# Performance work log

Measured on AMD Instinct MI355X. Metric: run time of the kernel, lower is better.

The kernel has to match this reference:

```python
import jax, jax.numpy as jnp
import numpy as np

HEADS = 12
HEAD_SIZE = 64
NEG_BIG = 1e12


def _rope_sin_cos(seq_len, head_size, dtype):
    # embeddings[n, 2i] = sin(n * 10000^(-2i/d)), [n, 2i+1] = cos(...)
    pos = jnp.arange(seq_len, dtype=dtype)                      # [s]
    idx = jnp.arange(head_size // 2, dtype=dtype)               # [d/2]
    inv_freq = jnp.power(jnp.asarray(10000.0, dtype), -2.0 * idx / head_size)
    ang = jnp.einsum('n,d->nd', pos, inv_freq)                  # [s, d/2]
    # cos_pos / sin_pos: repeat_interleave each frequency twice -> [1, s, 1, d]
    cos = jnp.repeat(jnp.cos(ang), 2, axis=-1)[None, :, None, :]
    sin = jnp.repeat(jnp.sin(ang), 2, axis=-1)[None, :, None, :]
    return sin, cos


def _rotate_half_interleaved(x):
    # stack([-x[..., 1::2], x[..., ::2]], -1).reshape_as(x)
    x2 = jnp.stack([-x[..., 1::2], x[..., ::2]], axis=-1)
    return x2.reshape(x.shape)


def setup_inputs() -> dict:
    key = jax.random.key(0)
    k1, k2 = jax.random.split(key)
    bs, s, h = 16, 512, 768
    hidden = jax.random.normal(k1, (bs, s, h), dtype=jnp.float32)
    attention_mask = jnp.ones((bs, s), dtype=jnp.int32)
    W = jax.random.normal(k2, (h, HEADS * 2 * HEAD_SIZE), dtype=jnp.float32) * (h ** -0.5)
    b = jnp.zeros((HEADS * 2 * HEAD_SIZE,), dtype=jnp.float32)
    return {"hidden": hidden, "attention_mask": attention_mask, "W": W, "b": b}


def reference(hidden, attention_mask, W, b):
    bs, s, _ = hidden.shape
    x = hidden @ W + b                                           # [b, s, heads*2*hd]
    x = x.reshape(bs, s, HEADS, 2, HEAD_SIZE)
    qw, kw = x[..., 0, :], x[..., 1, :]                          # [b, s, h, d]

    sin, cos = _rope_sin_cos(s, HEAD_SIZE, hidden.dtype)
    qw = qw * cos + _rotate_half_interleaved(qw) * sin
    kw = kw * cos + _rotate_half_interleaved(kw) * sin

    logits = jnp.einsum('bmhd,bnhd->bhmn', qw, kw)               # [b, h, s, s]

    am = attention_mask.astype(logits.dtype)
    pad_mask = 1.0 - am[:, None, None, :] * am[:, None, :, None]
    logits = logits - pad_mask * NEG_BIG

    tril = jnp.tril(jnp.ones((s, s), dtype=logits.dtype), k=-1)  # strictly lower
    logits = logits - tril[None, None, :, :] * NEG_BIG

    return logits / (HEAD_SIZE ** 0.5)
```

## Files before the change

### kernel.cpp

```cpp
#include <hip/hip_runtime.h>
#include <math.h>

#define HEADS 12
#define HSZ   64
#define SEQ   512
#define HID   768
#define NOUT  1536
#define NEGQ  1.25e11f

typedef _Float16 f16x8 __attribute__((ext_vector_type(8)));
typedef _Float16 f16x4 __attribute__((ext_vector_type(4)));
typedef float    f32x4 __attribute__((ext_vector_type(4)));
typedef int      i32x4 __attribute__((ext_vector_type(4)));
typedef int      i32x8 __attribute__((ext_vector_type(8)));

__device__ __forceinline__ void async_ld16(const void* g, void* l) {
  __builtin_amdgcn_global_load_lds(
      (__attribute__((address_space(1))) void*)g,
      (__attribute__((address_space(3))) void*)l, 16, 0, 0);
}

__global__ __launch_bounds__(256) void prep_k(
    const float* __restrict__ hidden, const float* __restrict__ W,
    unsigned char* __restrict__ Xb8, unsigned char* __restrict__ Wt8,
    float2* __restrict__ tab)
{
  __shared__ float t_lds[32][33];
  const int b = blockIdx.x;
  const int t = threadIdx.x;
  if (b < 1152) {
    const int tk = b % 24, tn = b / 24;
    const int k0 = tk * 32, n0 = tn * 32;
    const int tx = t & 31, ty = t >> 5;
#pragma unroll
    for (int r = 0; r < 4; ++r)
      t_lds[ty + r * 8][tx] = W[(size_t)(k0 + ty + r * 8) * NOUT + n0 + tx];
    __syncthreads();
    const int nl = t >> 3, kg = t & 7;
    int w = __builtin_amdgcn_cvt_pk_fp8_f32(t_lds[kg * 4 + 0][nl],
                                            t_lds[kg * 4 + 1][nl], 0, false);
    w = __builtin_amdgcn_cvt_pk_fp8_f32(t_lds[kg * 4 + 2][nl],
                                        t_lds[kg * 4 + 3][nl], w, true);
    *(int*)&Wt8[(size_t)(n0 + nl) * HID + k0 + kg * 4] = w;
  } else if (b < 1152 + 1536) {
    const int base = (b - 1152) * 1024;
    const float4* src4 = (const float4*)hidden;
    int* dst = (int*)Xb8;
#pragma unroll
    for (int p = 0; p < 4; ++p) {
      const int i = base + p * 256 + t;
      const float4 v = src4[i];
      int o = __builtin_amdgcn_cvt_pk_fp8_f32(v.x, v.y, 0, false);
      o = __builtin_amdgcn_cvt_pk_fp8_f32(v.z, v.w, o, true);
      dst[i] = o;
    }
  } else {
    const int e = (b - 2688) * 256 + t;
    const int si = e >> 5, fi = e & 31;
    float inv = powf(10000.f, -(float)fi / 32.f);
    float ang = (float)si * inv;
    float sv, cv;
    sincosf(ang, &sv, &cv);
    tab[e] = make_float2(cv, sv);
  }
}

__global__ __launch_bounds__(256) void gemm1_k(
    const unsigned char* __restrict__ Xb8, const unsigned char* __restrict__ Wt8,
    const float* __restrict__ bias, const float2* __restrict__ tab,
    const int* __restrict__ am, float* __restrict__ out,
    _Float16* __restrict__ qb, _Float16* __restrict__ kb)
{
  __shared__ __align__(16) int As4[4096];
  __shared__ __align__(16) int Bs4[4096];
  const int tid = threadIdx.x;
  const int blk = blockIdx.x;

  if (blk >= 768) {
    const int idx = blk - 768;
    const int bh = idx / 6, f = idx % 6;
    const int te = (0xEDC984 >> (f * 4)) & 15;
    const int m0 = (te >> 2) * 128, n0 = (te & 3) * 128;
    const int* amb = am + (bh / HEADS) * SEQ;
    float* obase = out + (size_t)bh * SEQ * SEQ;
#pragma unroll
    for (int p = 0; p < 16; ++p) {
      const int ff = p * 256 + tid;
      const int row = ff >> 5, c4 = (ff & 31) * 4;
      const int m = m0 + row;
      const float amm = (float)amb[m];
      const int nb = n0 + c4;
      const int4 a4 = *(const int4*)&amb[nb];
      f32x4 v;
      v[0] = -(2.f - amm * (float)a4.x) * NEGQ;
      v[1] = -(2.f - amm * (float)a4.y) * NEGQ;
      v[2] = -(2.f - amm * (float)a4.z) * NEGQ;
      v[3] = -(2.f - amm * (float)a4.w) * NEGQ;
      __builtin_nontemporal_store(v, (f32x4*)&obase[(size_t)m * SEQ + nb]);
    }
    return;
  }

  const int lane = tid & 63;
  const int m0 = (blk & 63) * 128;
  const int h = blk >> 6;
  const int n0 = h * 128;
  const int wm = ((tid >> 6) & 1) * 64;
  const int wn = (tid >> 7) * 64;
  const int lrow = lane & 15;
  const int q = lane >> 4;

  f32x4 acc[4][4] = {};

#pragma unroll
  for (int c = 0; c < 4; ++c) {
    const int s = tid + c * 256;
    const int row = s >> 3, cc = s & 7;
    const int so = (((cc >> 1) ^ (row & 3)) << 5) + ((cc & 1) << 4);
    async_ld16(Xb8 + (size_t)(m0 + row) * HID + so, (char*)As4 + s * 16);
    async_ld16(Wt8 + (size_t)(n0 + row) * HID + so, (char*)Bs4 + s * 16);
  }

  for (int kt = 0; kt < 6; ++kt) {
    __syncthreads();
    i32x8 af[4], bf[4];
#pragma unroll
    for (int i = 0; i < 4; ++i) {
      const int ra = wm + i * 16 + lrow;
      const int oa = ra * 32 + ((q ^ (ra & 3)) << 3);
      i32x4 lo = *(const i32x4*)&As4[oa];
      i32x4 hi = *(const i32x4*)&As4[oa + 4];
      af[i] = (i32x8){lo.x, lo.y, lo.z, lo.w, hi.x, hi.y, hi.z, hi.w};
      const int rb = wn + i * 16 + lrow;
      const int ob = rb * 32 + ((q ^ (rb & 3)) << 3);
      lo = *(const i32x4*)&Bs4[ob];
      hi = *(const i32x4*)&Bs4[ob + 4];
      bf[i] = (i32x8){lo.x, lo.y, lo.z, lo.w, hi.x, hi.y, hi.z, hi.w};
    }
    __syncthreads();
    if (kt < 5) {
      const int kbase = (kt + 1) * 128;
#pragma unroll
      for (int c = 0; c < 4; ++c) {
        const int s = tid + c * 256;
        const int row = s >> 3, cc = s & 7;
        const int so = (((cc >> 1) ^ (row & 3)) << 5) + ((cc & 1) << 4);
        async_ld16(Xb8 + (size_t)(m0 + row) * HID + kbase + so, (char*)As4 + s * 16);
        async_ld16(Wt8 + (size_t)(n0 + row) * HID + kbase + so, (char*)Bs4 + s * 16);
      }
    }
#pragma unroll
    for (int i = 0; i < 4; ++i)
#pragma unroll
      for (int j = 0; j < 4; ++j)
        acc[i][j] = __builtin_amdgcn_mfma_scale_f32_16x16x128_f8f6f4(
            bf[j], af[i], acc[i][j], 0, 0,
            0, 0x7F7F7F7F, 0, 0x7F7F7F7F);
  }
  __syncthreads();

  {
    const int qlane = lane >> 4;
    const int rbase = wm + (lane & 15);
    f16x4* sdst = wn ? (f16x4*)Bs4 : (f16x4*)As4;
#pragma unroll
    for (int j = 0; j < 4; ++j) {
      const int d0 = j * 16 + qlane * 4;
      const int nb = n0 + wn + d0;
      const float4 b4 = *(const float4*)&bias[nb];
      const int fi0 = d0 >> 1;
#pragma unroll
      for (int i = 0; i < 4; ++i) {
        const int r = rbase + i * 16;
        const int m = m0 + r;
        const int si = m & (SEQ - 1);
        const float4 cs = *(const float4*)&tab[si * 32 + fi0];
        const float v0 = acc[i][j][0] + b4.x;
        const float v1 = acc[i][j][1] + b4.y;
        const float v2 = acc[i][j][2] + b4.z;
        const float v3 = acc[i][j][3] + b4.w;
        f16x4 o;
        o.x = (_Float16)fmaf(v0, cs.x, -v1 * cs.y);
        o.y = (_Float16)fmaf(v1, cs.x, v0 * cs.y);
        o.z = (_Float16)fmaf(v2, cs.z, -v3 * cs.w);
        o.w = (_Float16)fmaf(v3, cs.z, v2 * cs.w);
        sdst[r * 16 + ((d0 >> 2) ^ ((r & 7) << 1))] = o;
      }
    }
  }
  __syncthreads();

  {
    const int bb = m0 >> 9;
    const int si0 = m0 & (SEQ - 1);
    _Float16* qdst = qb + ((size_t)(bb * HEADS + h) * SEQ + si0) * HSZ;
    _Float16* kdst = kb + ((size_t)(bb * HEADS + h) * SEQ + si0) * HSZ;
#pragma unroll
    for (int p = 0; p < 4; ++p) {
      const int idx = p * 256 + tid;
      const int row = idx >> 3, v = idx & 7;
      const int sv = v ^ (row & 7);
      f16x8 qv = ((const f16x8*)As4)[row * 8 + sv];
      f16x8 kv = ((const f16x8*)Bs4)[row * 8 + sv];
      *(f16x8*)(qdst + row * HSZ + v * 8) = qv;
      *(f16x8*)(kdst + row * HSZ + v * 8) = kv;
    }
  }
}

__global__ __launch_bounds__(256) void gemm2_k(
    const _Float16* __restrict__ qb, const _Float16* __restrict__ kb,
    const int* __restrict__ am, float* __restrict__ out)
{
  __shared__ __align__(16) float sbuf[64 * 128];
  const int tid = threadIdx.x;
  const int blk = blockIdx.x;
  const int xcd = blk & 7;
  const int slot = blk >> 3;
  const int bh = xcd * 24 + slot / 10;
  const int bb = bh / HEADS;
  const int te = (int)((0xFBA7653210ULL >> ((slot % 10) * 4)) & 15);
  const int mt = te >> 2, nt = te & 3;
  const int m0 = mt * 128, n0 = nt * 128;
  const int* amb = am + bb * SEQ;
  float* obase = out + (size_t)bh * SEQ * SEQ;

  const _Float16* qg = qb + (size_t)bh * SEQ * HSZ;
  const _Float16* kg = kb + (size_t)bh * SEQ * HSZ;
  const int lane = tid & 63;
  const int wm = ((tid >> 6) & 1) * 64;
  const int wn = (tid >> 7) * 64;
  const int lrow = lane & 15;
  const int lk = (lane >> 4) * 8;

  f16x8 af[4][2], bf[4][2];
#pragma unroll
  for (int i = 0; i < 4; ++i)
#pragma unroll
    for (int h = 0; h < 2; ++h) {
      af[i][h] = *(const f16x8*)(qg + (size_t)(m0 + wm + i * 16 + lrow) * HSZ + h * 32 + lk);
      bf[i][h] = *(const f16x8*)(kg + (size_t)(n0 + wn + i * 16 + lrow) * HSZ + h * 32 + lk);
    }

  f32x4 acc[4][4] = {};
#pragma unroll
  for (int h = 0; h < 2; ++h)
#pragma unroll
    for (int i = 0; i < 4; ++i)
#pragma unroll
      for (int j = 0; j < 4; ++j)
        acc[i][j] = __builtin_amdgcn_mfma_f32_16x16x32_f16(bf[j][h], af[i][h], acc[i][j], 0, 0, 0);

  const int qlane = lane >> 4;
  const int rloc = lane & 15;
  const int wmp = wm >> 6;
  for (int ph = 0; ph < 2; ++ph) {
    if (wmp == ph) {
#pragma unroll
      for (int i = 0; i < 4; ++i) {
        const int r = i * 16 + rloc;
        const int m = m0 + wm + r;
        const float amm = (float)amb[m];
#pragma unroll
        for (int j = 0; j < 4; ++j) {
          const int nb = n0 + wn + j * 16 + qlane * 4;
          const int4 a4 = *(const int4*)&amb[nb];
          f32x4 v;
          v[0] = fmaf(acc[i][j][0], 0.125f,
                      -((float)(nb + 0 < m) + (1.f - amm * (float)a4.x)) * NEGQ);
          v[1] = fmaf(acc[i][j][1], 0.125f,
                      -((float)(nb + 1 < m) + (1.f - amm * (float)a4.y)) * NEGQ);
          v[2] = fmaf(acc[i][j][2], 0.125f,
                      -((float)(nb + 2 < m) + (1.f - amm * (float)a4.z)) * NEGQ);
          v[3] = fmaf(acc[i][j][3], 0.125f,
                      -((float)(nb + 3 < m) + (1.f - amm * (float)a4.w)) * NEGQ);
          const int t = ((wn >> 2) + j * 4 + qlane) ^ (r & 7);
          *(f32x4*)&sbuf[r * 128 + t * 4] = v;
        }
      }
    }
    __syncthreads();
    const int rowbase = m0 + ph * 64;
#pragma unroll
    for (int p = 0; p < 8; ++p) {
      const int idx = p * 256 + tid;
      const int row = idx >> 5, t = idx & 31;
      f32x4 v = *(const f32x4*)&sbuf[row * 128 + ((t ^ (row & 7)) * 4)];
      __builtin_nontemporal_store(
          v, (f32x4*)&obase[(size_t)(rowbase + row) * SEQ + n0 + t * 4]);
    }
    __syncthreads();
  }
}

extern "C" void kernel_launch(void* const* d_in, const int* in_sizes, int n_in,
                              void* d_out, int out_size, void* d_ws, size_t ws_size,
                              hipStream_t stream) {
  const float* hidden = (const float*)d_in[0];
  const int*   am     = (const int*)d_in[1];
  const float* W      = (const float*)d_in[2];
  const float* bias   = (const float*)d_in[3];
  float* out = (float*)d_out;
  char* ws = (char*)d_ws;
  unsigned char* Xb8 = (unsigned char*)(ws);
  unsigned char* Wt8 = (unsigned char*)(ws + 6291456);
  _Float16* qb = (_Float16*)(ws + 7471104);
  _Float16* kb = (_Float16*)(ws + 20054016);
  float2*   tab = (float2*)(ws + 32636928);

  prep_k<<<dim3(2752), dim3(256), 0, stream>>>(hidden, W, Xb8, Wt8, tab);
  gemm1_k<<<dim3(1920), dim3(256), 0, stream>>>(Xb8, Wt8, bias, tab, am, out, qb, kb);
  gemm2_k<<<dim3(1920), dim3(256), 0, stream>>>(qb, kb, am, out);
}
```

Before: 255.7 us.

## Compute diagonal logit tiles inside gemm1 from on-chip Q/K, shrink gemm2 grid

After gemm1 writes the rotated Q and K tile to shared memory, each block now computes the diagonal 128x128 logits tile straight from shared memory, applying the mask and scale, and stores it through a swizzled LDS staging buffer. gemm2 then only handles the remaining six upper-triangle off-diagonal tiles per head, so its grid drops from 1920 to 1152 blocks. This removes a re-read of Q/K from global memory and some launch work, but adds MFMA and epilogue time to the tail of each gemm1 block and extra syncs.

Measured after the change: 268.8 us. 5.1% more time.

```diff
diff --git a/kernel.cpp b/kernel.cpp
--- a/kernel.cpp
+++ b/kernel.cpp
@@ -71,8 +71,9 @@
     const int* __restrict__ am, float* __restrict__ out,
     _Float16* __restrict__ qb, _Float16* __restrict__ kb)
 {
-  __shared__ __align__(16) int As4[4096];
-  __shared__ __align__(16) int Bs4[4096];
+  __shared__ __align__(16) int shm[8192];
+  int* As4 = shm;
+  int* Bs4 = shm + 4096;
   const int tid = threadIdx.x;
   const int blk = blockIdx.x;
 
@@ -102,7 +103,8 @@
   }
 
   const int lane = tid & 63;
-  const int m0 = (blk & 63) * 128;
+  const int mi = blk & 63;
+  const int m0 = mi * 128;
   const int h = blk >> 6;
   const int n0 = h * 128;
   const int wm = ((tid >> 6) & 1) * 64;
@@ -206,6 +208,79 @@
       *(f16x8*)(kdst + row * HSZ + v * 8) = kv;
     }
   }
+
+  const int bb2 = mi >> 2;
+  const int m0d = (mi & 3) * 128;
+  const int* amb = am + bb2 * SEQ;
+  float* obase = out + (size_t)(bb2 * HEADS + h) * SEQ * SEQ;
+
+  f16x8 af2[4][2], bf2[4][2];
+  {
+    const f16x8* q16 = (const f16x8*)As4;
+    const f16x8* k16 = (const f16x8*)Bs4;
+#pragma unroll
+    for (int i = 0; i < 4; ++i)
+#pragma unroll
+      for (int hh = 0; hh < 2; ++hh) {
+        const int rA = wm + i * 16 + lrow;
+        af2[i][hh] = q16[rA * 8 + ((hh * 4 + q) ^ (rA & 7))];
+        const int rB = wn + i * 16 + lrow;
+        bf2[i][hh] = k16[rB * 8 + ((hh * 4 + q) ^ (rB & 7))];
+      }
+  }
+
+  f32x4 acc2[4][4] = {};
+#pragma unroll
+  for (int hh = 0; hh < 2; ++hh)
+#pragma unroll
+    for (int i = 0; i < 4; ++i)
+#pragma unroll
+      for (int j = 0; j < 4; ++j)
+        acc2[i][j] = __builtin_amdgcn_mfma_f32_16x16x32_f16(
+            bf2[j][hh], af2[i][hh], acc2[i][j], 0, 0, 0);
+
+  __syncthreads();
+  float* sbuf = (float*)shm;
+  const int qlane = lane >> 4;
+  const int rloc = lane & 15;
+  const int wmp = wm >> 6;
+  for (int ph = 0; ph < 2; ++ph) {
+    if (wmp == ph) {
+#pragma unroll
+      for (int i = 0; i < 4; ++i) {
+        const int r = i * 16 + rloc;
+        const int m = m0d + wm + r;
+        const float amm = (float)amb[m];
+#pragma unroll
+        for (int j = 0; j < 4; ++j) {
+          const int nb = m0d + wn + j * 16 + qlane * 4;
+          const int4 a4 = *(const int4*)&amb[nb];
+          f32x4 v;
+          v[0] = fmaf(acc2[i][j][0], 0.125f,
+                      -((float)(nb + 0 < m) + (1.f - amm * (float)a4.x)) * NEGQ);
+          v[1] = fmaf(acc2[i][j][1], 0.125f,
+                      -((float)(nb + 1 < m) + (1.f - amm * (float)a4.y)) * NEGQ);
+          v[2] = fmaf(acc2[i][j][2], 0.125f,
+                      -((float)(nb + 2 < m) + (1.f - amm * (float)a4.z)) * NEGQ);
+          v[3] = fmaf(acc2[i][j][3], 0.125f,
+                      -((float)(nb + 3 < m) + (1.f - amm * (float)a4.w)) * NEGQ);
+          const int t = ((wn >> 2) + j * 4 + qlane) ^ (r & 7);
+          *(f32x4*)&sbuf[r * 128 + t * 4] = v;
+        }
+      }
+    }
+    __syncthreads();
+    const int rowbase = m0d + ph * 64;
+#pragma unroll
+    for (int p = 0; p < 8; ++p) {
+      const int idx = p * 256 + tid;
+      const int row = idx >> 5, t = idx & 31;
+      f32x4 v = *(const f32x4*)&sbuf[row * 128 + ((t ^ (row & 7)) * 4)];
+      __builtin_nontemporal_store(
+          v, (f32x4*)&obase[(size_t)(rowbase + row) * SEQ + m0d + t * 4]);
+    }
+    __syncthreads();
+  }
 }
 
 __global__ __launch_bounds__(256) void gemm2_k(
@@ -217,9 +292,9 @@
   const int blk = blockIdx.x;
   const int xcd = blk & 7;
   const int slot = blk >> 3;
-  const int bh = xcd * 24 + slot / 10;
+  const int bh = xcd * 24 + slot / 6;
   const int bb = bh / HEADS;
-  const int te = (int)((0xFBA7653210ULL >> ((slot % 10) * 4)) & 15);
+  const int te = (0xB76321 >> ((slot % 6) * 4)) & 15;
   const int mt = te >> 2, nt = te & 3;
   const int m0 = mt * 128, n0 = nt * 128;
   const int* amb = am + bb * SEQ;
@@ -310,5 +385,5 @@
 
   prep_k<<<dim3(2752), dim3(256), 0, stream>>>(hidden, W, Xb8, Wt8, tab);
   gemm1_k<<<dim3(1920), dim3(256), 0, stream>>>(Xb8, Wt8, bias, tab, am, out, qb, kb);
-  gemm2_k<<<dim3(1920), dim3(256), 0, stream>>>(qb, kb, am, out);
-}
+  gemm2_k<<<dim3(1152), dim3(256), 0, stream>>>(qb, kb, am, out);
+}
```
